# Performance work log

Measured on AMD Instinct MI355X. Metric: run time of the kernel, lower is better.

## Reference

```python
import jax, jax.numpy as jnp
import numpy as np

N_ENT = 4096
N_REL = 4
F = 128
BATCH = 8192
ADJ_DENSITY = 0.01


def setup_inputs() -> dict:
    key = jax.random.key(0)
    ks = jax.random.split(key, 8)
    features = jax.random.normal(ks[0], (N_ENT, F), dtype=jnp.float32)
    # sparse binary adjacency per relation (matches count_nonzero degree normalization)
    adj = (jax.random.uniform(ks[1], (N_REL, N_ENT, N_ENT)) < ADJ_DENSITY).astype(jnp.float32)
    W1 = jax.random.normal(ks[2], (N_REL, F, F), dtype=jnp.float32)  # [R, out, in]
    W2 = jax.random.normal(ks[3], (N_REL, F, F), dtype=jnp.float32)
    # DistMult init: diagonal relation matrices (full params, as in the torch code)
    diag_vals = jax.random.normal(ks[4], (N_REL, F), dtype=jnp.float32)
    relmats = jax.vmap(jnp.diag)(diag_vals)  # [R, F, F]
    e1_idx = jax.random.randint(ks[5], (BATCH,), 0, N_ENT)
    rel_idx = jax.random.randint(ks[6], (BATCH,), 0, N_REL)
    e2_idx = jax.random.randint(ks[7], (BATCH,), 0, N_ENT)
    return {"features": features, "adj": adj, "W1": W1, "W2": W2,
            "relmats": relmats, "e1_idx": e1_idx, "rel_idx": rel_idx, "e2_idx": e2_idx}


def _conv_layer(adj, feat, W):
    # degree normalization: 1 / count_nonzero(A_r, dim=1), zeros -> 1
    deg = jnp.sum(adj != 0, axis=2).astype(feat.dtype)            # [R, N]
    inv_deg = 1.0 / jnp.where(deg == 0, 1.0, deg)                 # [R, N]
    agg = jnp.einsum('rnm,mf->rnf', adj, feat)                    # [R, N, F_in]
    y = jnp.einsum('rnf,rof->rno', agg, W)                        # [R, N, F_out] (x @ W_r.T)
    y = jnp.sum(inv_deg[:, :, None] * y, axis=0)                  # [N, F_out]
    return jax.nn.sigmoid(y)


def reference(features, adj, W1, W2, relmats, e1_idx, rel_idx, e2_idx):
    h = _conv_layer(adj, features, W1)
    h = _conv_layer(adj, h, W2)
    # DistMult scores: pred[r] = h @ M_r @ h.T  -> [R, N, N]
    pred = jnp.einsum('nf,rfg,mg->rnm', h, relmats, h)
    # per-sample scalar gather pred[rel][e1][e2]
    return pred[rel_idx, e1_idx, e2_idx]
```

## Files before the change

kernel.cpp:

```cpp
#include <hip/hip_runtime.h>
#include <hip/hip_bf16.h>

#define N_ENT 4096
#define N_REL 4
#define FDIM 128
#define KDIM 512
#define MAXNZ 128
#define BATCH 8192
#define NROWS (N_REL * N_ENT)

__global__ __launch_bounds__(256) void k_prep(
    const float* __restrict__ W1, const float* __restrict__ W2,
    const float* __restrict__ M, const float* __restrict__ adj,
    const float* __restrict__ feat,
    float* __restrict__ W1T, float* __restrict__ W2T, float* __restrict__ diagM,
    unsigned short* __restrict__ cols, int* __restrict__ cnt,
    float* __restrict__ inv_deg, float* __restrict__ agg) {
  int blk = blockIdx.x;
  if (blk < NROWS) {
    int row = blk;
    int r = row >> 12;
    int node = row & (N_ENT - 1);
    __shared__ unsigned short sc[MAXNZ];
    __shared__ float part[8][FDIM];
    __shared__ int lcnt;
    if (threadIdx.x == 0) lcnt = 0;
    __syncthreads();
    const float4* src = (const float4*)(adj + (size_t)row * N_ENT);
    int base = threadIdx.x * 16;
    unsigned mask = 0;
#pragma unroll
    for (int q = 0; q < 4; ++q) {
      float4 v = src[threadIdx.x * 4 + q];
      if (v.x != 0.f) mask |= 1u << (q * 4 + 0);
      if (v.y != 0.f) mask |= 1u << (q * 4 + 1);
      if (v.z != 0.f) mask |= 1u << (q * 4 + 2);
      if (v.w != 0.f) mask |= 1u << (q * 4 + 3);
    }
    int mycnt = __popc(mask);
    int p = 0;
    if (mycnt) p = atomicAdd(&lcnt, mycnt);
    while (mask) {
      int b = __ffs(mask) - 1;
      mask &= mask - 1;
      if (p < MAXNZ) sc[p] = (unsigned short)(base + b);
      ++p;
    }
    __syncthreads();
    int c = lcnt; if (c > MAXNZ) c = MAXNZ;
    float w = 1.0f / (float)(c > 0 ? c : 1);
    if (threadIdx.x < c) cols[(size_t)row * MAXNZ + threadIdx.x] = sc[threadIdx.x];
    if (threadIdx.x == 0) { cnt[row] = c; inv_deg[row] = w; }
    int l = threadIdx.x & 31;
    int g = threadIdx.x >> 5;
    const float* fp = feat + l * 4;
    float ax = 0.f, ay = 0.f, az = 0.f, aw = 0.f;
    for (int j = g; j < c; j += 8) {
      float4 v = *(const float4*)(fp + (int)sc[j] * FDIM);
      ax += v.x; ay += v.y; az += v.z; aw += v.w;
    }
    part[g][l * 4 + 0] = ax; part[g][l * 4 + 1] = ay;
    part[g][l * 4 + 2] = az; part[g][l * 4 + 3] = aw;
    __syncthreads();
    if (g == 0) {
      float sx = 0.f, sy = 0.f, sz = 0.f, sw2 = 0.f;
#pragma unroll
      for (int gg = 0; gg < 8; ++gg) {
        sx += part[gg][l * 4 + 0]; sy += part[gg][l * 4 + 1];
        sz += part[gg][l * 4 + 2]; sw2 += part[gg][l * 4 + 3];
      }
      float4 res; res.x = sx * w; res.y = sy * w; res.z = sz * w; res.w = sw2 * w;
      *(float4*)(agg + (size_t)node * KDIM + r * FDIM + l * 4) = res;
    }
    return;
  }
  int ab = blk - NROWS;
  if (ab < 512) {
    int id = ab * 256 + threadIdx.x;
    int which = id >> 16;
    int e = id & 65535;
    int rr = e >> 14, rem = e & 16383, ff = rem >> 7, o = rem & 127;
    const float* srcw = which ? W2 : W1;
    float* dst = which ? W2T : W1T;
    dst[e] = srcw[(rr * FDIM + o) * FDIM + ff];
    return;
  }
  int idx = (ab - 512) * 256 + threadIdx.x;
  int rr = idx >> 7, ff = idx & 127;
  diagM[idx] = M[((size_t)(rr * FDIM + ff)) * FDIM + ff];
}

__device__ __forceinline__ void gemm_body(
    const float* __restrict__ A, const float* __restrict__ B,
    float* __restrict__ C, int n0, float (*red)[128]) {
  constexpr int KD = KDIM, KH = KDIM / 2, Ncol = FDIM;
  int o = threadIdx.x & 127;
  int half = threadIdx.x >> 7;
  const float* Ap = A + (size_t)n0 * KD + half * KH;
  const float* Bp = B + (size_t)half * KH * Ncol + o;
  float acc[8] = {0.f, 0.f, 0.f, 0.f, 0.f, 0.f, 0.f, 0.f};
#pragma unroll 2
  for (int k = 0; k < KH; k += 4) {
    float4 a0 = *(const float4*)(Ap + 0 * KD + k);
    float4 a1 = *(const float4*)(Ap + 1 * KD + k);
    float4 a2 = *(const float4*)(Ap + 2 * KD + k);
    float4 a3 = *(const float4*)(Ap + 3 * KD + k);
    float4 a4 = *(const float4*)(Ap + 4 * KD + k);
    float4 a5 = *(const float4*)(Ap + 5 * KD + k);
    float4 a6 = *(const float4*)(Ap + 6 * KD + k);
    float4 a7 = *(const float4*)(Ap + 7 * KD + k);
    float b0 = Bp[(size_t)(k + 0) * Ncol];
    float b1 = Bp[(size_t)(k + 1) * Ncol];
    float b2 = Bp[(size_t)(k + 2) * Ncol];
    float b3 = Bp[(size_t)(k + 3) * Ncol];
    acc[0] += a0.x * b0 + a0.y * b1 + a0.z * b2 + a0.w * b3;
    acc[1] += a1.x * b0 + a1.y * b1 + a1.z * b2 + a1.w * b3;
    acc[2] += a2.x * b0 + a2.y * b1 + a2.z * b2 + a2.w * b3;
    acc[3] += a3.x * b0 + a3.y * b1 + a3.z * b2 + a3.w * b3;
    acc[4] += a4.x * b0 + a4.y * b1 + a4.z * b2 + a4.w * b3;
    acc[5] += a5.x * b0 + a5.y * b1 + a5.z * b2 + a5.w * b3;
    acc[6] += a6.x * b0 + a6.y * b1 + a6.z * b2 + a6.w * b3;
    acc[7] += a7.x * b0 + a7.y * b1 + a7.z * b2 + a7.w * b3;
  }
  if (half) {
#pragma unroll
    for (int i = 0; i < 8; ++i) red[i][o] = acc[i];
  }
  __syncthreads();
  if (!half) {
#pragma unroll
    for (int i = 0; i < 8; ++i) {
      float v = acc[i] + red[i][o];
      v = 1.f / (1.f + __expf(-v));
      C[(size_t)(n0 + i) * Ncol + o] = v;
    }
  }
}

__global__ __launch_bounds__(256) void k_gemm(
    const float* __restrict__ A, const float* __restrict__ B,
    float* __restrict__ C) {
  __shared__ float red[8][128];
  gemm_body(A, B, C, blockIdx.x * 8, red);
}

__global__ __launch_bounds__(256) void k_layer2(
    const unsigned short* __restrict__ cols, const int* __restrict__ cnt,
    const float* __restrict__ inv_deg, const float* __restrict__ h1,
    const float* __restrict__ W2T, float* __restrict__ agg,
    float* __restrict__ h2) {
  int n0 = blockIdx.x * 8;
  __shared__ unsigned short lc[8][N_REL][MAXNZ];
  __shared__ float red[8][128];
  {
    int i = threadIdx.x >> 3;
    int t8 = threadIdx.x & 7;
    int nb = i >> 2, r = i & 3;
    int row = r * N_ENT + n0 + nb;
    int c = cnt[row];
    for (int j = t8; j < c; j += 8)
      lc[nb][r][j] = cols[(size_t)row * MAXNZ + j];
  }
  __syncthreads();
  {
    int l = threadIdx.x & 31;
    int g = threadIdx.x >> 5;
    const float* fp = h1 + l * 4;
#pragma unroll
    for (int q = 0; q < 4; ++q) {
      int pair = g + q * 8;
      int nb = pair >> 2, r = pair & 3;
      int row = r * N_ENT + n0 + nb;
      int c = cnt[row];
      float w = inv_deg[row];
      float ax = 0.f, ay = 0.f, az = 0.f, aw = 0.f;
      int j = 0;
      for (; j + 2 <= c; j += 2) {
        float4 v0 = *(const float4*)(fp + (int)lc[nb][r][j] * FDIM);
        float4 v1 = *(const float4*)(fp + (int)lc[nb][r][j + 1] * FDIM);
        ax += v0.x + v1.x; ay += v0.y + v1.y;
        az += v0.z + v1.z; aw += v0.w + v1.w;
      }
      if (j < c) {
        float4 v = *(const float4*)(fp + (int)lc[nb][r][j] * FDIM);
        ax += v.x; ay += v.y; az += v.z; aw += v.w;
      }
      float4 res; res.x = ax * w; res.y = ay * w; res.z = az * w; res.w = aw * w;
      *(float4*)(agg + (size_t)(n0 + nb) * KDIM + r * FDIM + l * 4) = res;
    }
  }
  __syncthreads();
  gemm_body(agg, W2T, h2, n0, red);
}

__global__ __launch_bounds__(256) void k_score(
    const float* __restrict__ h, const float* __restrict__ diagM,
    const int* __restrict__ e1, const int* __restrict__ rel,
    const int* __restrict__ e2, float* __restrict__ out) {
  int wave = threadIdx.x >> 6;
  int lane = threadIdx.x & 63;
  int b = blockIdx.x * 4 + wave;
  int a = e1[b], r = rel[b], c = e2[b];
  const float* hp = h + (size_t)a * FDIM;
  const float* dp = diagM + (size_t)r * FDIM;
  const float* gp = h + (size_t)c * FDIM;
  float v = hp[lane] * dp[lane] * gp[lane]
          + hp[lane + 64] * dp[lane + 64] * gp[lane + 64];
#pragma unroll
  for (int off = 32; off > 0; off >>= 1) v += __shfl_down(v, off, 64);
  if (lane == 0) out[b] = v;
}

extern "C" void kernel_launch(void* const* d_in, const int* in_sizes, int n_in,
                              void* d_out, int out_size, void* d_ws, size_t ws_size,
                              hipStream_t stream) {
  const float* feat = (const float*)d_in[0];
  const float* adj  = (const float*)d_in[1];
  const float* W1   = (const float*)d_in[2];
  const float* W2   = (const float*)d_in[3];
  const float* M    = (const float*)d_in[4];
  const int* e1     = (const int*)d_in[5];
  const int* rel    = (const int*)d_in[6];
  const int* e2     = (const int*)d_in[7];
  float* out = (float*)d_out;

  char* ws = (char*)d_ws;
  unsigned short* cols = (unsigned short*)(ws);
  int*   cnt  = (int*)  (ws + 4194304);
  float* inv  = (float*)(ws + 4259840);
  float* W1T  = (float*)(ws + 4325376);
  float* W2T  = (float*)(ws + 4587520);
  float* dM   = (float*)(ws + 4849664);
  float* agg  = (float*)(ws + 5111808);
  float* h1   = (float*)(ws + 13500416);
  float* h2   = (float*)(ws + 15597568);

  k_prep<<<NROWS + 514, 256, 0, stream>>>(
      W1, W2, M, adj, feat, W1T, W2T, dM, cols, cnt, inv, agg);

  k_gemm<<<N_ENT / 8, 256, 0, stream>>>(agg, W1T, h1);
  k_layer2<<<N_ENT / 8, 256, 0, stream>>>(cols, cnt, inv, h1, W2T, agg, h2);
  k_score<<<BATCH / 4, 256, 0, stream>>>(h2, dM, e1, rel, e2, out);
}
```

Baseline: 461.4 us.

## Stream adjacency with nontemporal loads and keep layer-2 aggregation in LDS

The adjacency scan now uses nontemporal loads, so the 268MB dense adjacency does not evict useful data from cache. The prep gather loop is unrolled by two, and the final reduction is spread over 128 threads instead of 32. Layer 2 now processes 4 nodes per block and keeps the aggregated features in shared memory instead of writing and rereading global agg, which doubles the block count. The trade-off is that each block reuses every W2T load across only 4 rows instead of 8, so weight traffic doubles.

Result: no change. 463.0 us (+0.4%).

```diff
diff --git a/kernel.cpp b/kernel.cpp
--- a/kernel.cpp
+++ b/kernel.cpp
@@ -8,6 +8,8 @@
 #define MAXNZ 128
 #define BATCH 8192
 #define NROWS (N_REL * N_ENT)
+
+typedef float f4v __attribute__((ext_vector_type(4)));
 
 __global__ __launch_bounds__(256) void k_prep(
     const float* __restrict__ W1, const float* __restrict__ W2,
@@ -26,12 +28,12 @@
     __shared__ int lcnt;
     if (threadIdx.x == 0) lcnt = 0;
     __syncthreads();
-    const float4* src = (const float4*)(adj + (size_t)row * N_ENT);
+    const f4v* src = (const f4v*)(adj + (size_t)row * N_ENT);
     int base = threadIdx.x * 16;
     unsigned mask = 0;
 #pragma unroll
     for (int q = 0; q < 4; ++q) {
-      float4 v = src[threadIdx.x * 4 + q];
+      f4v v = __builtin_nontemporal_load(src + threadIdx.x * 4 + q);
       if (v.x != 0.f) mask |= 1u << (q * 4 + 0);
       if (v.y != 0.f) mask |= 1u << (q * 4 + 1);
       if (v.z != 0.f) mask |= 1u << (q * 4 + 2);
@@ -55,22 +57,25 @@
     int g = threadIdx.x >> 5;
     const float* fp = feat + l * 4;
     float ax = 0.f, ay = 0.f, az = 0.f, aw = 0.f;
-    for (int j = g; j < c; j += 8) {
+    int j = g;
+    for (; j + 8 < c; j += 16) {
+      float4 v0 = *(const float4*)(fp + (int)sc[j] * FDIM);
+      float4 v1 = *(const float4*)(fp + (int)sc[j + 8] * FDIM);
+      ax += v0.x + v1.x; ay += v0.y + v1.y;
+      az += v0.z + v1.z; aw += v0.w + v1.w;
+    }
+    if (j < c) {
       float4 v = *(const float4*)(fp + (int)sc[j] * FDIM);
       ax += v.x; ay += v.y; az += v.z; aw += v.w;
     }
     part[g][l * 4 + 0] = ax; part[g][l * 4 + 1] = ay;
     part[g][l * 4 + 2] = az; part[g][l * 4 + 3] = aw;
     __syncthreads();
-    if (g == 0) {
-      float sx = 0.f, sy = 0.f, sz = 0.f, sw2 = 0.f;
-#pragma unroll
-      for (int gg = 0; gg < 8; ++gg) {
-        sx += part[gg][l * 4 + 0]; sy += part[gg][l * 4 + 1];
-        sz += part[gg][l * 4 + 2]; sw2 += part[gg][l * 4 + 3];
-      }
-      float4 res; res.x = sx * w; res.y = sy * w; res.z = sz * w; res.w = sw2 * w;
-      *(float4*)(agg + (size_t)node * KDIM + r * FDIM + l * 4) = res;
+    if (threadIdx.x < FDIM) {
+      float s = 0.f;
+#pragma unroll
+      for (int gg = 0; gg < 8; ++gg) s += part[gg][threadIdx.x];
+      agg[(size_t)node * KDIM + r * FDIM + threadIdx.x] = s * w;
     }
     return;
   }
@@ -147,18 +152,18 @@
 __global__ __launch_bounds__(256) void k_layer2(
     const unsigned short* __restrict__ cols, const int* __restrict__ cnt,
     const float* __restrict__ inv_deg, const float* __restrict__ h1,
-    const float* __restrict__ W2T, float* __restrict__ agg,
-    float* __restrict__ h2) {
-  int n0 = blockIdx.x * 8;
-  __shared__ unsigned short lc[8][N_REL][MAXNZ];
-  __shared__ float red[8][128];
+    const float* __restrict__ W2T, float* __restrict__ h2) {
+  int n0 = blockIdx.x * 4;
+  __shared__ unsigned short lc[4][N_REL][MAXNZ];
+  __shared__ __align__(16) float aggL[4][KDIM];
+  __shared__ float red[4][128];
   {
-    int i = threadIdx.x >> 3;
-    int t8 = threadIdx.x & 7;
+    int i = threadIdx.x >> 4;
+    int t16 = threadIdx.x & 15;
     int nb = i >> 2, r = i & 3;
     int row = r * N_ENT + n0 + nb;
     int c = cnt[row];
-    for (int j = t8; j < c; j += 8)
+    for (int j = t16; j < c; j += 16)
       lc[nb][r][j] = cols[(size_t)row * MAXNZ + j];
   }
   __syncthreads();
@@ -167,7 +172,7 @@
     int g = threadIdx.x >> 5;
     const float* fp = h1 + l * 4;
 #pragma unroll
-    for (int q = 0; q < 4; ++q) {
+    for (int q = 0; q < 2; ++q) {
       int pair = g + q * 8;
       int nb = pair >> 2, r = pair & 3;
       int row = r * N_ENT + n0 + nb;
@@ -186,11 +191,46 @@
         ax += v.x; ay += v.y; az += v.z; aw += v.w;
       }
       float4 res; res.x = ax * w; res.y = ay * w; res.z = az * w; res.w = aw * w;
-      *(float4*)(agg + (size_t)(n0 + nb) * KDIM + r * FDIM + l * 4) = res;
+      *(float4*)&aggL[nb][r * FDIM + l * 4] = res;
     }
   }
   __syncthreads();
-  gemm_body(agg, W2T, h2, n0, red);
+  {
+    constexpr int KH = KDIM / 2, Ncol = FDIM;
+    int o = threadIdx.x & 127;
+    int half = threadIdx.x >> 7;
+    const float* Bp = W2T + (size_t)half * KH * Ncol + o;
+    int kbase = half * KH;
+    float acc[4] = {0.f, 0.f, 0.f, 0.f};
+#pragma unroll 2
+    for (int k = 0; k < KH; k += 4) {
+      float4 a0 = *(const float4*)&aggL[0][kbase + k];
+      float4 a1 = *(const float4*)&aggL[1][kbase + k];
+      float4 a2 = *(const float4*)&aggL[2][kbase + k];
+      float4 a3 = *(const float4*)&aggL[3][kbase + k];
+      float b0 = Bp[(size_t)(k + 0) * Ncol];
+      float b1 = Bp[(size_t)(k + 1) * Ncol];
+      float b2 = Bp[(size_t)(k + 2) * Ncol];
+      float b3 = Bp[(size_t)(k + 3) * Ncol];
+      acc[0] += a0.x * b0 + a0.y * b1 + a0.z * b2 + a0.w * b3;
+      acc[1] += a1.x * b0 + a1.y * b1 + a1.z * b2 + a1.w * b3;
+      acc[2] += a2.x * b0 + a2.y * b1 + a2.z * b2 + a2.w * b3;
+      acc[3] += a3.x * b0 + a3.y * b1 + a3.z * b2 + a3.w * b3;
+    }
+    if (half) {
+#pragma unroll
+      for (int i = 0; i < 4; ++i) red[i][o] = acc[i];
+    }
+    __syncthreads();
+    if (!half) {
+#pragma unroll
+      for (int i = 0; i < 4; ++i) {
+        float v = acc[i] + red[i][o];
+        v = 1.f / (1.f + __expf(-v));
+        h2[(size_t)(n0 + i) * Ncol + o] = v;
+      }
+    }
+  }
 }
 
 __global__ __launch_bounds__(256) void k_score(
@@ -239,6 +279,6 @@
       W1, W2, M, adj, feat, W1T, W2T, dM, cols, cnt, inv, agg);
 
   k_gemm<<<N_ENT / 8, 256, 0, stream>>>(agg, W1T, h1);
-  k_layer2<<<N_ENT / 8, 256, 0, stream>>>(cols, cnt, inv, h1, W2T, agg, h2);
+  k_layer2<<<N_ENT / 4, 256, 0, stream>>>(cols, cnt, inv, h1, W2T, h2);
   k_score<<<BATCH / 4, 256, 0, stream>>>(h2, dM, e1, rel, e2, out);
 }
```
